# Kernel tuning notes

Hardware: AMD Instinct MI355X
Metric: run time of the kernel (lower is better)

## Reference

```python
import jax, jax.numpy as jnp
import numpy as np

_BIG = 1e4  # kornia uses 1e4 as the 'infinity' for masked-out kernel positions


def _windows(img, pad_val):
    """Return the 9 shifted 3x3 neighborhoods of img, stacked on axis 0.
    img: [B,C,H,W] -> [9,B,C,H,W]. Border padded with pad_val so padded
    pixels never win the min (erosion) / max (dilation), matching kornia.
    """
    B, C, H, W = img.shape
    p = jnp.pad(img, ((0, 0), (0, 0), (1, 1), (1, 1)), constant_values=pad_val)
    return jnp.stack([p[..., i:i + H, j:j + W]
                      for i in range(3) for j in range(3)], axis=0)


def _erosion(img, mask):
    w = _windows(img, _BIG)
    return jnp.min(jnp.where(mask, w, _BIG), axis=0)


def _dilation(img, mask):
    w = _windows(img, -_BIG)
    return jnp.max(jnp.where(mask, w, -_BIG), axis=0)


def setup_inputs() -> dict:
    key = jax.random.key(0)
    img = jax.random.uniform(key, (8, 3, 1024, 1024), dtype=jnp.float32)
    # kernel0: symmetric 3x3 cross structuring element
    kernel = jnp.array([[0, 1, 0], [1, 1, 1], [0, 1, 0]], dtype=jnp.int32)
    return {"img": img, "kernel": kernel}


def reference(img, kernel):
    # morphological opening = erosion followed by dilation, same structuring element
    mask = (kernel.reshape(9, 1, 1, 1, 1) == 1)
    eroded = _erosion(img, mask)
    opened = _dilation(eroded, mask)
    return opened
```

## Files before the change

kernel.cpp:

```cpp
#include <hip/hip_runtime.h>
#include <stdint.h>

#define BIGV 1e4f

constexpr int RH    = 8;
constexpr int NSLOT = 5;
constexpr int WROW  = 1024;

struct Row { float2 L; float4 M; float2 R; };
struct Ero { float eL; float4 eM; float eR; };

#define WAITVM(n)  asm volatile("s_waitcnt vmcnt(" #n ")" ::: "memory")
#define WAITALL0() asm volatile("s_waitcnt vmcnt(0) lgkmcnt(0)" ::: "memory")
#define WAITLG0()  asm volatile("s_waitcnt lgkmcnt(0)" ::: "memory")
#define SCHED0()   __builtin_amdgcn_sched_barrier(0)

__device__ __forceinline__ float min3f(float a, float b, float c) { return fminf(fminf(a, b), c); }
__device__ __forceinline__ float max3f(float a, float b, float c) { return fmaxf(fmaxf(a, b), c); }

__device__ __forceinline__ void gld16(const void* g, void* l) {
    __builtin_amdgcn_global_load_lds(
        (const __attribute__((address_space(1))) void*)g,
        (__attribute__((address_space(3))) void*)l, 16, 0, 0);
}

__device__ __forceinline__ void dma_row(const float* __restrict__ img, float* lds,
                                        int slot, int r, int H, int W, int lx) {
    const int rc = min(max(r, 0), H - 1);
    const float* src = img + (size_t)rc * W + 4 * lx;
    float* dst = lds + slot * WROW;
#pragma unroll
    for (int c = 0; c < 4; ++c)
        gld16(src + c * 256, dst + c * 256);
}

__device__ __forceinline__ void read_row4(const float* lds, int slot, int lx,
                                          int r, int H, Row* w) {
    if (r >= 0 && r < H) {
        const float* sb = lds + slot * WROW;
#pragma unroll
        for (int c = 0; c < 4; ++c) {
            const int fb = c * 256 + 4 * lx;
            w[c].M = *(const float4*)(sb + fb);
            if (c == 0 && lx == 0) w[c].L = make_float2(BIGV, BIGV);
            else                   w[c].L = *(const float2*)(sb + fb - 2);
            if (c == 3 && lx == 63) w[c].R = make_float2(BIGV, BIGV);
            else                    w[c].R = *(const float2*)(sb + fb + 4);
        }
    } else {
#pragma unroll
        for (int c = 0; c < 4; ++c) {
            w[c].L = make_float2(BIGV, BIGV);
            w[c].M = make_float4(BIGV, BIGV, BIGV, BIGV);
            w[c].R = make_float2(BIGV, BIGV);
        }
    }
}

__device__ __forceinline__ float rget(const Row& r, int q) {
    switch (q) {
        case -2: return r.L.x; case -1: return r.L.y;
        case 0:  return r.M.x; case 1:  return r.M.y;
        case 2:  return r.M.z; case 3:  return r.M.w;
        case 4:  return r.R.x; default: return r.R.y;
    }
}
__device__ __forceinline__ float eget(const Ero& e, int q) {
    switch (q) {
        case -1: return e.eL;
        case 0:  return e.eM.x; case 1:  return e.eM.y;
        case 2:  return e.eM.z; case 3:  return e.eM.w;
        default: return e.eR;
    }
}

__device__ __forceinline__ Ero erode_cross(const Row& a, const Row& b, const Row& c,
                                           int r, int H, int gx, int W) {
    Ero e;
    if (r >= 0 && r < H) {
        e.eL   = min3f(min3f(a.L.y, b.L.y, c.L.y), b.L.x, b.M.x);
        e.eM.x = min3f(min3f(a.M.x, b.M.x, c.M.x), b.L.y, b.M.y);
        e.eM.y = min3f(min3f(a.M.y, b.M.y, c.M.y), b.M.x, b.M.z);
        e.eM.z = min3f(min3f(a.M.z, b.M.z, c.M.z), b.M.y, b.M.w);
        e.eM.w = min3f(min3f(a.M.w, b.M.w, c.M.w), b.M.z, b.R.x);
        e.eR   = min3f(min3f(a.R.x, b.R.x, c.R.x), b.M.w, b.R.y);
        if (gx == 0)     e.eL = -BIGV;
        if (gx + 4 >= W) e.eR = -BIGV;
    } else {
        e.eL = -BIGV; e.eM = make_float4(-BIGV, -BIGV, -BIGV, -BIGV); e.eR = -BIGV;
    }
    return e;
}

__device__ __forceinline__ float4 dilate_cross(const Ero& t, const Ero& m, const Ero& b) {
    float4 o;
    o.x = max3f(max3f(t.eM.x, m.eM.x, b.eM.x), m.eL,   m.eM.y);
    o.y = max3f(max3f(t.eM.y, m.eM.y, b.eM.y), m.eM.x, m.eM.z);
    o.z = max3f(max3f(t.eM.z, m.eM.z, b.eM.z), m.eM.y, m.eM.w);
    o.w = max3f(max3f(t.eM.w, m.eM.w, b.eM.w), m.eM.z, m.eR);
    return o;
}

__device__ __forceinline__ Ero erode_gen(const Row& a, const Row& b, const Row& c,
                                         const bool* m, int r, int H, int gx, int W) {
    Ero e;
    if (r >= 0 && r < H) {
        float v[6];
#pragma unroll
        for (int p = 0; p < 6; ++p) {
            float acc = BIGV;
#pragma unroll
            for (int k = 0; k < 9; ++k) {
                const int di = k / 3, dj = k % 3;
                const Row& rr = (di == 0) ? a : ((di == 1) ? b : c);
                float t = rget(rr, p - 2 + dj);
                acc = fminf(acc, m[k] ? t : BIGV);
            }
            v[p] = acc;
        }
        e.eL = v[0]; e.eM.x = v[1]; e.eM.y = v[2]; e.eM.z = v[3]; e.eM.w = v[4]; e.eR = v[5];
        if (gx == 0)     e.eL = -BIGV;
        if (gx + 4 >= W) e.eR = -BIGV;
    } else {
        e.eL = -BIGV; e.eM = make_float4(-BIGV, -BIGV, -BIGV, -BIGV); e.eR = -BIGV;
    }
    return e;
}

__device__ __forceinline__ float4 dilate_gen(const Ero& e0, const Ero& e1, const Ero& e2,
                                             const bool* m) {
    float o[4];
#pragma unroll
    for (int j = 0; j < 4; ++j) {
        float acc = -BIGV;
#pragma unroll
        for (int k = 0; k < 9; ++k) {
            const int di = k / 3, dj = k % 3;
            const Ero& ee = (di == 0) ? e0 : ((di == 1) ? e1 : e2);
            acc = fmaxf(acc, m[k] ? eget(ee, j + dj - 1) : -BIGV);
        }
        o[j] = acc;
    }
    return make_float4(o[0], o[1], o[2], o[3]);
}

template <bool CROSS>
__device__ __forceinline__ void run(const float* __restrict__ img, float* __restrict__ out,
                                    float* lds, const bool* m, int y0, int lx, int H, int W) {
    WAITALL0();
#pragma unroll
    for (int k = 0; k < NSLOT; ++k) dma_row(img, lds, k, y0 - 2 + k, H, W, lx);
    SCHED0();
    WAITVM(4);
    SCHED0();
    Row B[4], C[4], Cur[4], Nxt[4];
    read_row4(lds, 0, lx, y0 - 2, H, B);
    read_row4(lds, 1, lx, y0 - 1, H, C);
    read_row4(lds, 2, lx, y0,     H, Cur);
    read_row4(lds, 3, lx, y0 + 1, H, Nxt);
    WAITLG0();
    SCHED0();
    dma_row(img, lds, 0, y0 + 3, H, W, lx);
    dma_row(img, lds, 1, y0 + 4, H, W, lx);
    dma_row(img, lds, 2, y0 + 5, H, W, lx);
    SCHED0();
    Ero E0[4], E1[4];
#pragma unroll
    for (int c = 0; c < 4; ++c) {
        const int gx = c * 256 + 4 * lx;
        E0[c] = CROSS ? erode_cross(B[c], C[c], Cur[c], y0 - 1, H, gx, W)
                      : erode_gen (B[c], C[c], Cur[c], m, y0 - 1, H, gx, W);
        E1[c] = CROSS ? erode_cross(C[c], Cur[c], Nxt[c], y0, H, gx, W)
                      : erode_gen (C[c], Cur[c], Nxt[c], m, y0, H, gx, W);
    }

#pragma unroll
    for (int i = 0; i < RH; ++i) {
        const int y = y0 + i;
        if      (i == 0) WAITVM(12);
        else if (i == 1) WAITVM(16);
        else if (i == 2) WAITVM(20);
        else if (i == 3) WAITVM(24);
        else if (i == 4) WAITVM(24);
        else if (i == 5) WAITVM(20);
        else if (i == 6) WAITVM(16);
        else             WAITVM(12);
        SCHED0();
        Row N[4];
        read_row4(lds, (i + 4) % NSLOT, lx, y + 2, H, N);
#pragma unroll
        for (int c = 0; c < 4; ++c) {
            const int gx = c * 256 + 4 * lx;
            Ero E2 = CROSS ? erode_cross(Cur[c], Nxt[c], N[c], y + 1, H, gx, W)
                           : erode_gen (Cur[c], Nxt[c], N[c], m, y + 1, H, gx, W);
            float4 o = CROSS ? dilate_cross(E0[c], E1[c], E2)
                             : dilate_gen (E0[c], E1[c], E2, m);
            *(float4*)(out + (size_t)y * W + gx) = o;
            E0[c] = E1[c]; E1[c] = E2;
            Cur[c] = Nxt[c]; Nxt[c] = N[c];
        }
        SCHED0();
        if (i < RH - 4) {
            dma_row(img, lds, (i + 3) % NSLOT, y + 6, H, W, lx);
            SCHED0();
        }
    }
}

__global__ __launch_bounds__(64, 2) void opening_kernel(
    const float* __restrict__ img, const int* __restrict__ kern,
    float* __restrict__ out, int H, int W)
{
    __shared__ float lds[NSLOT * WROW];
    const int lx = threadIdx.x;

    const int bid   = blockIdx.x;
    const int chunk = gridDim.x >> 3;
    const int swz   = (bid & 7) * chunk + (bid >> 3);
    const int sy    = swz & 127;
    const int plane = swz >> 7;
    const int y0    = sy * RH;
    const size_t pbase = (size_t)plane * H * W;

    bool m[9];
#pragma unroll
    for (int k = 0; k < 9; ++k) m[k] = (kern[k] == 1);
    const bool cross = m[1] && m[3] && m[4] && m[5] && m[7] &&
                       !m[0] && !m[2] && !m[6] && !m[8];

    if (cross) run<true >(img + pbase, out + pbase, lds, m, y0, lx, H, W);
    else       run<false>(img + pbase, out + pbase, lds, m, y0, lx, H, W);
}

extern "C" void kernel_launch(void* const* d_in, const int* in_sizes, int n_in,
                              void* d_out, int out_size, void* d_ws, size_t ws_size,
                              hipStream_t stream) {
    const float* img  = (const float*)d_in[0];
    const int*   kern = (const int*)d_in[1];
    float*       out  = (float*)d_out;

    const int H = 1024, W = 1024;
    const int planes = in_sizes[0] / (H * W);

    dim3 block(64);
    dim3 grid((H / RH) * planes);
    opening_kernel<<<grid, block, 0, stream>>>(img, kern, out, H, W);
}
```

Before: 184.6 us.

## Split each row between two wavefronts with seam exchange and nontemporal stores

Each block now has two wavefronts, each handling half of a 1024-wide row strip with its own LDS ring buffer. Each wave fetches the two boundary pixels across the seam from global memory with a scalar float2 load. Output stores become nontemporal, and the grid is now 2D with the block-ID swizzle removed. The aim is more waves in flight and fewer per-thread registers per wave, to hide latency better. The cost is an extra seam load per row and vmcnt wait thresholds retuned by hand, which could be miscounted.

```diff
diff --git a/kernel.cpp b/kernel.cpp
--- a/kernel.cpp
+++ b/kernel.cpp
@@ -1,11 +1,12 @@
 #include <hip/hip_runtime.h>
-#include <stdint.h>
 
 #define BIGV 1e4f
 
 constexpr int RH    = 8;
 constexpr int NSLOT = 5;
-constexpr int WROW  = 1024;
+constexpr int HALF  = 512;
+
+typedef float f32x4 __attribute__((ext_vector_type(4)));
 
 struct Row { float2 L; float4 M; float2 R; };
 struct Ero { float eL; float4 eM; float eR; };
@@ -24,32 +25,22 @@
         (__attribute__((address_space(3))) void*)l, 16, 0, 0);
 }
 
-__device__ __forceinline__ void dma_row(const float* __restrict__ img, float* lds,
-                                        int slot, int r, int H, int W, int lx) {
-    const int rc = min(max(r, 0), H - 1);
-    const float* src = img + (size_t)rc * W + 4 * lx;
-    float* dst = lds + slot * WROW;
-#pragma unroll
-    for (int c = 0; c < 4; ++c)
-        gld16(src + c * 256, dst + c * 256);
-}
-
-__device__ __forceinline__ void read_row4(const float* lds, int slot, int lx,
-                                          int r, int H, Row* w) {
+__device__ __forceinline__ void read_row2(const float* wlds, int slot, int lx,
+                                          int r, int H, bool isleft, float2 seam, Row* w) {
     if (r >= 0 && r < H) {
-        const float* sb = lds + slot * WROW;
-#pragma unroll
-        for (int c = 0; c < 4; ++c) {
-            const int fb = c * 256 + 4 * lx;
+        const float* sb = wlds + slot * HALF;
+#pragma unroll
+        for (int c = 0; c < 2; ++c) {
+            const int fb = c * 256 + lx * 4;
             w[c].M = *(const float4*)(sb + fb);
-            if (c == 0 && lx == 0) w[c].L = make_float2(BIGV, BIGV);
-            else                   w[c].L = *(const float2*)(sb + fb - 2);
-            if (c == 3 && lx == 63) w[c].R = make_float2(BIGV, BIGV);
-            else                    w[c].R = *(const float2*)(sb + fb + 4);
-        }
+            w[c].L = *(const float2*)(sb + fb - 2);
+            w[c].R = *(const float2*)(sb + fb + 4);
+        }
+        if (lx == 0)  w[0].L = isleft ? make_float2(BIGV, BIGV) : seam;
+        if (lx == 63) w[1].R = isleft ? seam : make_float2(BIGV, BIGV);
     } else {
 #pragma unroll
-        for (int c = 0; c < 4; ++c) {
+        for (int c = 0; c < 2; ++c) {
             w[c].L = make_float2(BIGV, BIGV);
             w[c].M = make_float4(BIGV, BIGV, BIGV, BIGV);
             w[c].R = make_float2(BIGV, BIGV);
@@ -146,28 +137,44 @@
 
 template <bool CROSS>
 __device__ __forceinline__ void run(const float* __restrict__ img, float* __restrict__ out,
-                                    float* lds, const bool* m, int y0, int lx, int H, int W) {
+                                    float* wlds, const bool* m, int xoff, int y0,
+                                    int lx, int H, int W, bool isleft) {
+    const int seamoff = isleft ? HALF : HALF - 2;
+    float2 seam[NSLOT];
+
     WAITALL0();
-#pragma unroll
-    for (int k = 0; k < NSLOT; ++k) dma_row(img, lds, k, y0 - 2 + k, H, W, lx);
     SCHED0();
-    WAITVM(4);
+#pragma unroll
+    for (int k = 0; k < NSLOT; ++k) {
+        const int rc = min(max(y0 - 2 + k, 0), H - 1);
+        const float* sp = img + (size_t)rc * W;
+        gld16(sp + xoff + 4 * lx,       wlds + k * HALF);
+        gld16(sp + xoff + 256 + 4 * lx, wlds + k * HALF + 256);
+        seam[k] = *(const float2*)(sp + seamoff);
+        SCHED0();
+    }
+    WAITVM(3);
     SCHED0();
-    Row B[4], C[4], Cur[4], Nxt[4];
-    read_row4(lds, 0, lx, y0 - 2, H, B);
-    read_row4(lds, 1, lx, y0 - 1, H, C);
-    read_row4(lds, 2, lx, y0,     H, Cur);
-    read_row4(lds, 3, lx, y0 + 1, H, Nxt);
+    Row B[2], C[2], Cur[2], Nxt[2];
+    read_row2(wlds, 0, lx, y0 - 2, H, isleft, seam[0], B);
+    read_row2(wlds, 1, lx, y0 - 1, H, isleft, seam[1], C);
+    read_row2(wlds, 2, lx, y0,     H, isleft, seam[2], Cur);
+    read_row2(wlds, 3, lx, y0 + 1, H, isleft, seam[3], Nxt);
     WAITLG0();
     SCHED0();
-    dma_row(img, lds, 0, y0 + 3, H, W, lx);
-    dma_row(img, lds, 1, y0 + 4, H, W, lx);
-    dma_row(img, lds, 2, y0 + 5, H, W, lx);
-    SCHED0();
-    Ero E0[4], E1[4];
-#pragma unroll
-    for (int c = 0; c < 4; ++c) {
-        const int gx = c * 256 + 4 * lx;
+#pragma unroll
+    for (int k = 0; k < 3; ++k) {
+        const int rc = min(max(y0 + 3 + k, 0), H - 1);
+        const float* sp = img + (size_t)rc * W;
+        gld16(sp + xoff + 4 * lx,       wlds + k * HALF);
+        gld16(sp + xoff + 256 + 4 * lx, wlds + k * HALF + 256);
+        seam[k] = *(const float2*)(sp + seamoff);
+        SCHED0();
+    }
+    Ero E0[2], E1[2];
+#pragma unroll
+    for (int c = 0; c < 2; ++c) {
+        const int gx = xoff + c * 256 + lx * 4;
         E0[c] = CROSS ? erode_cross(B[c], C[c], Cur[c], y0 - 1, H, gx, W)
                       : erode_gen (B[c], C[c], Cur[c], m, y0 - 1, H, gx, W);
         E1[c] = CROSS ? erode_cross(C[c], Cur[c], Nxt[c], y0, H, gx, W)
@@ -177,50 +184,54 @@
 #pragma unroll
     for (int i = 0; i < RH; ++i) {
         const int y = y0 + i;
-        if      (i == 0) WAITVM(12);
-        else if (i == 1) WAITVM(16);
-        else if (i == 2) WAITVM(20);
-        else if (i == 3) WAITVM(24);
-        else if (i == 4) WAITVM(24);
-        else if (i == 5) WAITVM(20);
-        else if (i == 6) WAITVM(16);
-        else             WAITVM(12);
-        SCHED0();
-        Row N[4];
-        read_row4(lds, (i + 4) % NSLOT, lx, y + 2, H, N);
-#pragma unroll
-        for (int c = 0; c < 4; ++c) {
-            const int gx = c * 256 + 4 * lx;
+        SCHED0();
+        if      (i == 0) WAITVM(9);
+        else if (i == 1) WAITVM(11);
+        else if (i == 2) WAITVM(13);
+        else if (i == 3) WAITVM(15);
+        else if (i == 4) WAITVM(15);
+        else if (i == 5) WAITVM(12);
+        else if (i == 6) WAITVM(9);
+        else             WAITVM(6);
+        SCHED0();
+        Row N[2];
+        read_row2(wlds, (i + 4) % NSLOT, lx, y + 2, H, isleft, seam[(i + 4) % NSLOT], N);
+#pragma unroll
+        for (int c = 0; c < 2; ++c) {
+            const int gx = xoff + c * 256 + lx * 4;
             Ero E2 = CROSS ? erode_cross(Cur[c], Nxt[c], N[c], y + 1, H, gx, W)
                            : erode_gen (Cur[c], Nxt[c], N[c], m, y + 1, H, gx, W);
             float4 o = CROSS ? dilate_cross(E0[c], E1[c], E2)
                              : dilate_gen (E0[c], E1[c], E2, m);
-            *(float4*)(out + (size_t)y * W + gx) = o;
+            f32x4 ov; ov.x = o.x; ov.y = o.y; ov.z = o.z; ov.w = o.w;
+            __builtin_nontemporal_store(ov, (f32x4*)(out + (size_t)y * W + gx));
             E0[c] = E1[c]; E1[c] = E2;
             Cur[c] = Nxt[c]; Nxt[c] = N[c];
         }
-        SCHED0();
         if (i < RH - 4) {
-            dma_row(img, lds, (i + 3) % NSLOT, y + 6, H, W, lx);
             SCHED0();
-        }
-    }
-}
-
-__global__ __launch_bounds__(64, 2) void opening_kernel(
+            const int rc = min(max(y + 6, 0), H - 1);
+            const float* sp = img + (size_t)rc * W;
+            const int s = (i + 3) % NSLOT;
+            gld16(sp + xoff + 4 * lx,       wlds + s * HALF);
+            gld16(sp + xoff + 256 + 4 * lx, wlds + s * HALF + 256);
+            seam[s] = *(const float2*)(sp + seamoff);
+            SCHED0();
+        }
+    }
+}
+
+__global__ __launch_bounds__(128, 3) void opening_kernel(
     const float* __restrict__ img, const int* __restrict__ kern,
     float* __restrict__ out, int H, int W)
 {
-    __shared__ float lds[NSLOT * WROW];
-    const int lx = threadIdx.x;
-
-    const int bid   = blockIdx.x;
-    const int chunk = gridDim.x >> 3;
-    const int swz   = (bid & 7) * chunk + (bid >> 3);
-    const int sy    = swz & 127;
-    const int plane = swz >> 7;
-    const int y0    = sy * RH;
-    const size_t pbase = (size_t)plane * H * W;
+    __shared__ float lds[2 * NSLOT * HALF + 2];
+    const int lx   = threadIdx.x & 63;
+    const int wid  = threadIdx.x >> 6;
+    const int xoff = wid * HALF;
+    const int y0   = blockIdx.x * RH;
+    const size_t pbase = (size_t)blockIdx.y * H * W;
+    float* wlds = lds + 2 + wid * NSLOT * HALF;
 
     bool m[9];
 #pragma unroll
@@ -228,8 +239,8 @@
     const bool cross = m[1] && m[3] && m[4] && m[5] && m[7] &&
                        !m[0] && !m[2] && !m[6] && !m[8];
 
-    if (cross) run<true >(img + pbase, out + pbase, lds, m, y0, lx, H, W);
-    else       run<false>(img + pbase, out + pbase, lds, m, y0, lx, H, W);
+    if (cross) run<true >(img + pbase, out + pbase, wlds, m, xoff, y0, lx, H, W, wid == 0);
+    else       run<false>(img + pbase, out + pbase, wlds, m, xoff, y0, lx, H, W, wid == 0);
 }
 
 extern "C" void kernel_launch(void* const* d_in, const int* in_sizes, int n_in,
@@ -242,7 +253,7 @@
     const int H = 1024, W = 1024;
     const int planes = in_sizes[0] / (H * W);
 
-    dim3 block(64);
-    dim3 grid((H / RH) * planes);
+    dim3 block(128);
+    dim3 grid(H / RH, planes);
     opening_kernel<<<grid, block, 0, stream>>>(img, kern, out, H, W);
 }
```

Measured after the change: 193.8 us. 5.0% more time.
